# Performance work log

Measured on AMD Instinct MI355X. Metric: run time of the kernel, lower is better.

## Reference

```python
import jax, jax.numpy as jnp
import numpy as np

HIDDEN = 1024
HEADS = 16
HEAD_DIM = HIDDEN // HEADS
LN_EPS = 1e-6


def setup_inputs() -> dict:
    key = jax.random.key(0)
    ks = jax.random.split(key, 12)
    B, S, H = 2, 2048, HIDDEN
    s = 1.0 / np.sqrt(H)
    inp = {
        "hidden_states": jax.random.normal(ks[0], (B, S, H), dtype=jnp.float32),
        "attention_mask": jnp.ones((B, S), dtype=jnp.int32),
        "Wq": jax.random.normal(ks[1], (H, H), dtype=jnp.float32) * s,
        "bq": jax.random.normal(ks[2], (H,), dtype=jnp.float32) * 0.02,
        "Wk": jax.random.normal(ks[3], (H, H), dtype=jnp.float32) * s,
        "bk": jax.random.normal(ks[4], (H,), dtype=jnp.float32) * 0.02,
        "Wv": jax.random.normal(ks[5], (H, H), dtype=jnp.float32) * s,
        "bv": jax.random.normal(ks[6], (H,), dtype=jnp.float32) * 0.02,
        "Wo": jax.random.normal(ks[7], (H, H), dtype=jnp.float32) * s,
        "bo": jax.random.normal(ks[8], (H,), dtype=jnp.float32) * 0.02,
        "ln_g": jnp.ones((H,), dtype=jnp.float32),
        "ln_b": jnp.zeros((H,), dtype=jnp.float32),
    }
    return inp


def _split_heads(x):
    B, S, H = x.shape
    return x.reshape(B, S, HEADS, HEAD_DIM).transpose(0, 2, 1, 3)  # [B,h,S,d]


def reference(hidden_states, attention_mask, Wq, bq, Wk, bk, Wv, bv, Wo, bo, ln_g, ln_b):
    # torch nn.Linear: y = x @ W.T + b
    q = _split_heads(hidden_states @ Wq.T + bq)
    k = _split_heads(hidden_states @ Wk.T + bk)
    v = _split_heads(hidden_states @ Wv.T + bv)

    scores = jnp.einsum("bhqd,bhkd->bhqk", q, k) / np.sqrt(HEAD_DIM)
    # 2D mask path: [B,K] -> [B,1,1,K]; (1-mask)*-1e18 additive bias
    bias = (1.0 - attention_mask[:, None, None, :].astype(scores.dtype)) * -1e18
    probs = jax.nn.softmax(scores + bias, axis=-1)
    # dropout is identity in eval mode
    ctx = jnp.einsum("bhqk,bhkd->bhqd", probs, v)
    B, h, S, d = ctx.shape
    ctx = ctx.transpose(0, 2, 1, 3).reshape(B, S, h * d)

    out = ctx @ Wo.T + bo
    res = out + hidden_states
    mu = jnp.mean(res, axis=-1, keepdims=True)
    var = jnp.mean(jnp.square(res - mu), axis=-1, keepdims=True)
    return (res - mu) * jax.lax.rsqrt(var + LN_EPS) * ln_g + ln_b
```

## Files before the change

### kernel.cpp

```cpp
#include <hip/hip_runtime.h>
#include <hip/hip_bf16.h>

#define SEQ     2048
#define BATCH   2
#define HID     1024
#define NHEADS  16
#define HD      64
#define MTOT    4096
#define KVHALF  1024
#define LNEPS   1e-6f
#define L2E     1.4426950408889634f
#define SHIFT2  26.0f

typedef __bf16 bf16_t;
typedef bf16_t bf16x8 __attribute__((ext_vector_type(8)));
typedef bf16_t bf16x4 __attribute__((ext_vector_type(4)));
typedef short  short4v __attribute__((ext_vector_type(4)));
typedef float  floatx4 __attribute__((ext_vector_type(4)));

__device__ __forceinline__ floatx4 mfma16(bf16x8 a, bf16x8 b, floatx4 c) {
    return __builtin_amdgcn_mfma_f32_16x16x32_bf16(a, b, c, 0, 0, 0);
}
__device__ __forceinline__ floatx4 mfma16k16(bf16x4 a, bf16x4 b, floatx4 c) {
    short4v as = __builtin_bit_cast(short4v, a);
    short4v bs = __builtin_bit_cast(short4v, b);
    return __builtin_amdgcn_mfma_f32_16x16x16bf16_1k(as, bs, c, 0, 0, 0);
}
__device__ __forceinline__ bf16x8 ldg8(const bf16_t* p) { return *(const bf16x8*)p; }

__device__ __forceinline__ void glds16(const bf16_t* src, char* dst) {
    __builtin_amdgcn_global_load_lds(
        (const __attribute__((address_space(1))) unsigned int*)src,
        (__attribute__((address_space(3))) unsigned int*)dst, 16, 0, 0);
}

__device__ __forceinline__ void stage128x32(const bf16_t* __restrict__ g, int row_stride,
                                            int k0, bf16_t* lds, int wave, int lane)
{
#pragma unroll
    for (int j = 0; j < 2; j++) {
        const int rbase = wave * 32 + j * 16;
        const bf16_t* src = g + (size_t)(rbase + (lane >> 2)) * row_stride + k0 + (lane & 3) * 8;
        bf16_t* dst = lds + rbase * 32;
        __builtin_amdgcn_global_load_lds(
            (const __attribute__((address_space(1))) unsigned int*)src,
            (__attribute__((address_space(3))) unsigned int*)dst, 16, 0, 0);
    }
}
__device__ __forceinline__ void stage64x32(const bf16_t* __restrict__ g, int row_stride,
                                           int k0, bf16_t* lds, int wave, int lane)
{
    const int rbase = wave * 16;
    const bf16_t* src = g + (size_t)(rbase + (lane >> 2)) * row_stride + k0 + (lane & 3) * 8;
    bf16_t* dst = lds + rbase * 32;
    __builtin_amdgcn_global_load_lds(
        (const __attribute__((address_space(1))) unsigned int*)src,
        (__attribute__((address_space(3))) unsigned int*)dst, 16, 0, 0);
}

__global__ __launch_bounds__(256) void cvt_kernel(
    const float* sX, const float* sWq, const float* sWk, const float* sWv, const float* sWo,
    bf16_t* dX, bf16_t* dWq, bf16_t* dWk, bf16_t* dWv, bf16_t* dWo)
{
    const int z = blockIdx.z;
    const float* src; bf16_t* dst; int n;
    switch (z) {
        case 0:  src = sX;  dst = dX;  n = MTOT * HID; break;
        case 1:  src = sWq; dst = dWq; n = HID * HID;  break;
        case 2:  src = sWk; dst = dWk; n = HID * HID;  break;
        case 3:  src = sWv; dst = dWv; n = HID * HID;  break;
        default: src = sWo; dst = dWo; n = HID * HID;  break;
    }
    const int n4 = n >> 2;
    const int stride = gridDim.x * blockDim.x;
    for (int i = blockIdx.x * blockDim.x + threadIdx.x; i < n4; i += stride) {
        const float4 v = ((const float4*)src)[i];
        bf16_t o[4] = {(bf16_t)v.x, (bf16_t)v.y, (bf16_t)v.z, (bf16_t)v.w};
        *(unsigned long long*)(dst + 4 * i) = *(unsigned long long*)o;
    }
}

__global__ __launch_bounds__(256) void qkv_kernel(
    const bf16_t* __restrict__ X,
    const bf16_t* __restrict__ Wq, const float* __restrict__ bq,
    const bf16_t* __restrict__ Wk, const float* __restrict__ bk,
    const bf16_t* __restrict__ Wv, const float* __restrict__ bv,
    bf16_t* __restrict__ Qo, bf16_t* __restrict__ Ko, bf16_t* __restrict__ Vo)
{
    const int z = blockIdx.z;
    const bf16_t* W    = (z == 0) ? Wq : (z == 1) ? Wk : Wv;
    const float*  bias = (z == 0) ? bq : (z == 1) ? bk : bv;
    bf16_t*       out  = (z == 0) ? Qo : (z == 1) ? Ko : Vo;

    const int tid  = threadIdx.x;
    const int lane = tid & 63;
    const int wave = tid >> 6;
    const int l16  = lane & 15;
    const int quad = lane >> 4;
    const int m_blk = blockIdx.y * 128;
    const int n_blk = blockIdx.x * 128;
    const int m_w = (wave >> 1) * 64;
    const int n_w = (wave & 1) * 64;

    __shared__ __align__(16) char smem[18432];
    bf16_t* As = (bf16_t*)smem;
    bf16_t* Bs = (bf16_t*)(smem + 8192);

    floatx4 acc[4][4];
#pragma unroll
    for (int i = 0; i < 4; i++)
#pragma unroll
        for (int j = 0; j < 4; j++) acc[i][j] = (floatx4)0.0f;

    for (int k0 = 0; k0 < HID; k0 += 32) {
        __syncthreads();
        stage128x32(X + (size_t)m_blk * HID, HID, k0, As, wave, lane);
        stage128x32(W + (size_t)n_blk * HID, HID, k0, Bs, wave, lane);
        __syncthreads();

        bf16x8 a[4], b[4];
#pragma unroll
        for (int i = 0; i < 4; i++) a[i] = *(const bf16x8*)&As[(m_w + i * 16 + l16) * 32 + quad * 8];
#pragma unroll
        for (int j = 0; j < 4; j++) b[j] = *(const bf16x8*)&Bs[(n_w + j * 16 + l16) * 32 + quad * 8];
#pragma unroll
        for (int i = 0; i < 4; i++)
#pragma unroll
            for (int j = 0; j < 4; j++) acc[i][j] = mfma16(a[i], b[j], acc[i][j]);
    }
    __syncthreads();

    float bv_[4];
#pragma unroll
    for (int j = 0; j < 4; j++) bv_[j] = bias[n_blk + n_w + j * 16 + l16];

    bf16_t* Tw = (bf16_t*)(smem + wave * 4608);

    if (z != 2) {
        const float scale = (z == 0) ? 0.125f : 1.0f;
        const int hN = (n_blk + n_w) >> 6;
#pragma unroll
        for (int ih = 0; ih < 2; ih++) {
#pragma unroll
            for (int i2 = 0; i2 < 2; i2++) {
                const int i = ih * 2 + i2;
#pragma unroll
                for (int j = 0; j < 4; j++)
#pragma unroll
                    for (int r = 0; r < 4; r++)
                        Tw[(i2 * 16 + quad * 4 + r) * 72 + j * 16 + l16] =
                            (bf16_t)((acc[i][j][r] + bv_[j]) * scale);
            }
#pragma unroll
            for (int p = 0; p < 4; p++) {
                const int srow = p * 8 + (lane >> 3);
                const int col  = (lane & 7) * 8;
                bf16x8 v = *(const bf16x8*)&Tw[srow * 72 + col];
                const int m = m_blk + m_w + ih * 32 + srow;
                const int bb = m >> 11, s = m & (SEQ - 1);
                *(bf16x8*)&out[(((size_t)(bb * NHEADS + hN)) * SEQ + s) * HD + col] = v;
            }
        }
    } else {
        const int m0 = m_blk + m_w;
        const int bb = m0 >> 11, s0 = m0 & (SEQ - 1);
#pragma unroll
        for (int jh = 0; jh < 2; jh++) {
#pragma unroll
            for (int j2 = 0; j2 < 2; j2++) {
                const int j = jh * 2 + j2;
#pragma unroll
                for (int i = 0; i < 4; i++) {
                    bf16x4 pk;
#pragma unroll
                    for (int r = 0; r < 4; r++) pk[r] = (bf16_t)(acc[i][j][r] + bv_[j]);
                    *(bf16x4*)&Tw[(j2 * 16 + l16) * 72 + i * 16 + quad * 4] = pk;
                }
            }
#pragma unroll
            for (int p = 0; p < 4; p++) {
                const int srow = p * 8 + (lane >> 3);
                const int col  = (lane & 7) * 8;
                bf16x8 v = *(const bf16x8*)&Tw[srow * 72 + col];
                const int n = n_blk + n_w + jh * 32 + srow;
                const int h = n >> 6, d = n & 63;
                *(bf16x8*)&out[(((size_t)(bb * NHEADS + h)) * HD + d) * SEQ + s0 + col] = v;
            }
        }
    }
}

__global__ __launch_bounds__(512, 4) void attn_kernel(
    const bf16_t* __restrict__ Q, const bf16_t* __restrict__ K,
    const bf16_t* __restrict__ Vt, const int* __restrict__ mask,
    bf16_t* __restrict__ ctx)
{
    const int B   = blockIdx.x;
    const int xcd = B & 7;
    const int idx = B >> 3;
    const int bh  = xcd * 4 + (idx & 3);
    const int q0  = (idx >> 2) * 128;
    const int b   = bh >> 4;
    const int h   = bh & 15;
    const int tid  = threadIdx.x;
    const int wave = tid >> 6;
    const int wq   = wave & 3;
    const int kh   = wave >> 2;
    const int lane = tid & 63;
    const int l16  = lane & 15;
    const int quad = lane >> 4;
    const int r7   = l16 & 7;

    const bf16_t* Qh = Q  + (size_t)bh * SEQ * HD;
    const bf16_t* Kh = K  + (size_t)bh * SEQ * HD;
    const bf16_t* Vh = Vt + (size_t)bh * HD * SEQ;
    const int*    mk = mask + b * SEQ;

    __shared__ __align__(16) char smem[73728];
    char*  base  = smem + kh * 32768;
    char*  Kb0   = base;
    char*  Vb0   = base + 8192;
    char*  Kb1   = base + 16384;
    char*  Vb1   = base + 24576;
    float* bias2 = (float*)(smem + 65536);

    const int qw  = q0 + wq * 32;
    const int kvb = kh * KVHALF;

    const int srow = wq * 8 + (lane >> 3);
    const int cK   = lane & 7;
    const bf16_t* srcK = Kh + (size_t)(kvb + srow) * HD + ((cK ^ (srow & 7)) * 8);
    const bf16_t* srcV = Vh + (size_t)srow * SEQ + kvb + (((2 * cK) ^ (srow & 14)) * 4);
    const int dofs = wq * 1024;

    const int kb0 = l16 * 128 + (((quad    ) ^ r7) << 4);
    const int kb1 = l16 * 128 + (((4 + quad) ^ r7) << 4);

    glds16(srcK,                Kb0 + dofs);
    glds16(srcK + 32 * HD,      Kb0 + dofs + 4096);
    glds16(srcV,                Vb0 + dofs);
    glds16(srcV + 32 * SEQ,     Vb0 + dofs + 4096);
    for (int i = tid; i < SEQ; i += 512)
        bias2[i] = (mk[i] ? 0.0f : -1.0e30f) - SHIFT2;

    bf16x8 bQ[2][2];
#pragma unroll
    for (int qh = 0; qh < 2; qh++)
#pragma unroll
        for (int kc = 0; kc < 2; kc++)
            bQ[qh][kc] = ldg8(Qh + (size_t)(qw + qh * 16 + l16) * HD + kc * 32 + quad * 8);

    const bf16x4 onesA = {(bf16_t)1.0f, (bf16_t)1.0f, (bf16_t)1.0f, (bf16_t)1.0f};
    floatx4 O[2][4];
    floatx4 psA[2];
#pragma unroll
    for (int qh = 0; qh < 2; qh++) {
        psA[qh] = (floatx4)0.0f;
#pragma unroll
        for (int dt = 0; dt < 4; dt++) O[qh][dt] = (floatx4)0.0f;
    }

    __syncthreads();

#define STAGE(kt, KB, VB)                                            \
    do {                                                             \
        const bf16_t* sk_ = srcK + (size_t)(kt) * HD;                \
        const bf16_t* sv_ = srcV + (kt);                             \
        glds16(sk_,            (KB) + dofs);                         \
        glds16(sk_ + 32 * HD,  (KB) + dofs + 4096);                  \
        glds16(sv_,            (VB) + dofs);                         \
        glds16(sv_ + 32 * SEQ, (VB) + dofs + 4096);                  \
    } while (0)

#define COMPUTE(kt, KB, VB)                                                       \
    do {                                                                          \
        __builtin_amdgcn_s_setprio(1);                                            \
        _Pragma("unroll")                                                         \
        for (int kvt = 0; kvt < 4; kvt++) {                                       \
            bf16x8 aK0 = *(const bf16x8*)((KB) + kb0 + kvt * 2048);               \
            bf16x8 aK1 = *(const bf16x8*)((KB) + kb1 + kvt * 2048);               \
            const floatx4 ad = *(const floatx4*)&bias2[kvb + (kt) + kvt * 16 + quad * 4]; \
            bf16x4 pb[2];                                                         \
            _Pragma("unroll")                                                     \
            for (int qh = 0; qh < 2; qh++) {                                      \
                floatx4 s = (floatx4)0.0f;                                        \
                s = mfma16(aK0, bQ[qh][0], s);                                    \
                s = mfma16(aK1, bQ[qh][1], s);                                    \
                floatx4 p;                                                        \
                _Pragma("unroll")                                                 \
                for (int r = 0; r < 4; r++)                                       \
                    p[r] = __builtin_amdgcn_exp2f(fmaf(s[r], L2E, ad[r]));        \
                _Pragma("unroll")                                                 \
                for (int r = 0; r < 4; r++) pb[qh][r] = (bf16_t)p[r];             \
            }                                                                     \
            psA[0] = mfma16k16(onesA, pb[0], psA[0]);                             \
            psA[1] = mfma16k16(onesA, pb[1], psA[1]);                             \
            const int vofs = l16 * 128 + ((((kvt << 2) + quad) ^ (l16 & 14)) << 3); \
            _Pragma("unroll")                                                     \
            for (int dt = 0; dt < 4; dt++) {                                      \
                bf16x4 aV = *(const bf16x4*)((VB) + vofs + dt * 2048);            \
                O[0][dt] = mfma16k16(aV, pb[0], O[0][dt]);                        \
                O[1][dt] = mfma16k16(aV, pb[1], O[1][dt]);                        \
            }                                                                     \
        }                                                                         \
        __builtin_amdgcn_s_setprio(0);                                            \
    } while (0)

    for (int t = 0; t < 16; t += 2) {
        STAGE((t + 1) * 64, Kb1, Vb1);
        COMPUTE(t * 64, Kb0, Vb0);
        __syncthreads();
        if (t + 2 < 16) STAGE((t + 2) * 64, Kb0, Vb0);
        COMPUTE((t + 1) * 64, Kb1, Vb1);
        __syncthreads();
    }
#undef STAGE
#undef COMPUTE

    if (kh == 1) {
        float* mw = (float*)(smem + wq * 10240) + lane * 40;
#pragma unroll
        for (int qh = 0; qh < 2; qh++) {
#pragma unroll
            for (int dt = 0; dt < 4; dt++)
                *(floatx4*)(mw + qh * 16 + dt * 4) = O[qh][dt];
            *(floatx4*)(mw + 32 + qh * 4) = psA[qh];
        }
    }
    __syncthreads();
    if (kh == 1) return;

    {
        const float* mr = (const float*)(smem + wq * 10240) + lane * 40;
#pragma unroll
        for (int qh = 0; qh < 2; qh++) {
#pragma unroll
            for (int dt = 0; dt < 4; dt++)
                O[qh][dt] += *(const floatx4*)(mr + qh * 16 + dt * 4);
            psA[qh] += *(const floatx4*)(mr + 32 + qh * 4);
        }
    }

#pragma unroll
    for (int qh = 0; qh < 2; qh++) {
        const float su = psA[qh][0];
        const float linv = (su > 0.0f) ? 1.0f / su : 0.0f;

        bf16_t* Pw = (bf16_t*)(smem + wq * 10240 + qh * 2304);
#pragma unroll
        for (int dt = 0; dt < 4; dt++) {
            floatx4 o = O[qh][dt] * linv;
            bf16x4 pk;
#pragma unroll
            for (int r = 0; r < 4; r++) pk[r] = (bf16_t)o[r];
            *(bf16x4*)&Pw[l16 * 72 + dt * 16 + quad * 4] = pk;
        }
#pragma unroll
        for (int ch = 0; ch < 2; ch++) {
            const int cc  = ch * 64 + lane;
            const int row = cc >> 3;
            const int col = (cc & 7) * 8;
            bf16x8 vv = *(const bf16x8*)&Pw[row * 72 + col];
            *(bf16x8*)&ctx[((size_t)(b * SEQ + qw + qh * 16 + row)) * HID + h * 64 + col] = vv;
        }
    }
}

__global__ __launch_bounds__(256) void oproj_kernel(
    const bf16_t* __restrict__ C, const bf16_t* __restrict__ Wo,
    const float* __restrict__ bo, const float* __restrict__ X,
    float* __restrict__ res)
{
    const int tid  = threadIdx.x;
    const int lane = tid & 63;
    const int wave = tid >> 6;
    const int l16  = lane & 15;
    const int quad = lane >> 4;
    const int m_blk = blockIdx.y * 64;
    const int n_blk = blockIdx.x * 128;
    const int n_w   = wave * 32;

    __shared__ __align__(16) char smem[12288];
    bf16_t* As = (bf16_t*)smem;
    bf16_t* Bs = (bf16_t*)(smem + 4096);

    floatx4 acc[4][2];
#pragma unroll
    for (int i = 0; i < 4; i++)
#pragma unroll
        for (int j = 0; j < 2; j++) acc[i][j] = (floatx4)0.0f;

    for (int k0 = 0; k0 < HID; k0 += 32) {
        __syncthreads();
        stage64x32 (C  + (size_t)m_blk * HID, HID, k0, As, wave, lane);
        stage128x32(Wo + (size_t)n_blk * HID, HID, k0, Bs, wave, lane);
        __syncthreads();

        bf16x8 a[4], b[2];
#pragma unroll
        for (int i = 0; i < 4; i++) a[i] = *(const bf16x8*)&As[(i * 16 + l16) * 32 + quad * 8];
#pragma unroll
        for (int j = 0; j < 2; j++) b[j] = *(const bf16x8*)&Bs[(n_w + j * 16 + l16) * 32 + quad * 8];
#pragma unroll
        for (int i = 0; i < 4; i++)
#pragma unroll
            for (int j = 0; j < 2; j++) acc[i][j] = mfma16(a[i], b[j], acc[i][j]);
    }
    __syncthreads();

    float bv_[2];
#pragma unroll
    for (int j = 0; j < 2; j++) bv_[j] = bo[n_blk + n_w + j * 16 + l16];

    float* Tw = (float*)(smem + wave * 2304);
#pragma unroll
    for (int ch = 0; ch < 4; ch++) {
#pragma unroll
        for (int j = 0; j < 2; j++)
#pragma unroll
            for (int r = 0; r < 4; r++)
                Tw[(quad * 4 + r) * 36 + j * 16 + l16] = acc[ch][j][r] + bv_[j];
#pragma unroll
        for (int cc = 0; cc < 2; cc++) {
            const int idx = cc * 64 + lane;
            const int row = idx >> 3;
            const int col = (idx & 7) * 4;
            float4 v = *(const float4*)&Tw[row * 36 + col];
            const int m = m_blk + ch * 16 + row;
            const float4 xv = *(const float4*)&X[(size_t)m * HID + n_blk + n_w + col];
            v.x += xv.x; v.y += xv.y; v.z += xv.z; v.w += xv.w;
            *(float4*)&res[(size_t)m * HID + n_blk + n_w + col] = v;
        }
    }
}

__global__ __launch_bounds__(256) void ln_kernel(
    const float* __restrict__ res,
    const float* __restrict__ g, const float* __restrict__ be,
    float* __restrict__ out)
{
    __shared__ float red1[4], red2[4];
    const int row  = blockIdx.x;
    const int lane = threadIdx.x & 63;
    const int wave = threadIdx.x >> 6;
    const float4 v = ((const float4*)(res + (size_t)row * HID))[threadIdx.x];

    float s = v.x + v.y + v.z + v.w;
#pragma unroll
    for (int off = 1; off < 64; off <<= 1) s += __shfl_xor(s, off, 64);
    if (lane == 0) red1[wave] = s;
    __syncthreads();
    const float mu = (red1[0] + red1[1] + red1[2] + red1[3]) * (1.0f / HID);

    const float d0 = v.x - mu, d1 = v.y - mu, d2 = v.z - mu, d3 = v.w - mu;
    float ss = d0 * d0 + d1 * d1 + d2 * d2 + d3 * d3;
#pragma unroll
    for (int off = 1; off < 64; off <<= 1) ss += __shfl_xor(ss, off, 64);
    if (lane == 0) red2[wave] = ss;
    __syncthreads();
    const float var = (red2[0] + red2[1] + red2[2] + red2[3]) * (1.0f / HID);
    const float rstd = rsqrtf(var + LNEPS);

    const float4 gv = ((const float4*)g)[threadIdx.x];
    const float4 bv = ((const float4*)be)[threadIdx.x];
    float4 o;
    o.x = d0 * rstd * gv.x + bv.x;
    o.y = d1 * rstd * gv.y + bv.y;
    o.z = d2 * rstd * gv.z + bv.z;
    o.w = d3 * rstd * gv.w + bv.w;
    ((float4*)(out + (size_t)row * HID))[threadIdx.x] = o;
}

extern "C" void kernel_launch(void* const* d_in, const int* in_sizes, int n_in,
                              void* d_out, int out_size, void* d_ws, size_t ws_size,
                              hipStream_t stream)
{
    const float* X  = (const float*)d_in[0];
    const int* mask = (const int*)d_in[1];
    const float* Wq = (const float*)d_in[2];  const float* bq = (const float*)d_in[3];
    const float* Wk = (const float*)d_in[4];  const float* bk = (const float*)d_in[5];
    const float* Wv = (const float*)d_in[6];  const float* bv = (const float*)d_in[7];
    const float* Wo = (const float*)d_in[8];  const float* bo = (const float*)d_in[9];
    const float* g  = (const float*)d_in[10]; const float* be = (const float*)d_in[11];
    float* out = (float*)d_out;

    char* ws = (char*)d_ws;
    bf16_t* Qb  = (bf16_t*)(ws);
    bf16_t* Kb  = (bf16_t*)(ws + (8ull  << 20));
    bf16_t* Vb  = (bf16_t*)(ws + (16ull << 20));
    bf16_t* Cb  = (bf16_t*)(ws + (24ull << 20));
    float*  Rb  = (float*)(ws);
    bf16_t* Xc  = (bf16_t*)(ws + (32ull << 20));
    bf16_t* Wqc = (bf16_t*)(ws + (40ull << 20));
    bf16_t* Wkc = (bf16_t*)(ws + (42ull << 20));
    bf16_t* Wvc = (bf16_t*)(ws + (44ull << 20));
    bf16_t* Woc = (bf16_t*)(ws + (46ull << 20));

    cvt_kernel <<<dim3(512, 1, 5), 256, 0, stream>>>(X, Wq, Wk, Wv, Wo, Xc, Wqc, Wkc, Wvc, Woc);
    qkv_kernel <<<dim3(8, 32, 3), 256, 0, stream>>>(Xc, Wqc, bq, Wkc, bk, Wvc, bv, Qb, Kb, Vb);
    attn_kernel<<<dim3(512), 512, 0, stream>>>(Qb, Kb, Vb, mask, Cb);
    oproj_kernel<<<dim3(8, 64), 256, 0, stream>>>(Cb, Woc, bo, X, Rb);
    ln_kernel  <<<MTOT, 256, 0, stream>>>(Rb, g, be, out);
}
```

Before: 121.1 us.

## Drop intra-block split-KV in attention; four waves each scan full sequence

The attention kernel previously used 8 waves per block, with two groups each covering half of the KV range and merging partial O and row sums through shared memory. Now each block has 4 waves that each loop over the whole KV sequence, with smaller shared memory and no merge step. This removes the merge traffic and the extra barrier, and lowers LDS use per block. With the grid size unchanged, it halves the waves per CU and doubles the serial loop length, which risks losing latency hiding.

New measurement: 122.6 us. Within noise of the previous version (+1.2%).

```diff
diff --git a/kernel.cpp b/kernel.cpp
--- a/kernel.cpp
+++ b/kernel.cpp
@@ -7,7 +7,6 @@
 #define NHEADS  16
 #define HD      64
 #define MTOT    4096
-#define KVHALF  1024
 #define LNEPS   1e-6f
 #define L2E     1.4426950408889634f
 #define SHIFT2  26.0f
@@ -190,7 +189,7 @@
     }
 }
 
-__global__ __launch_bounds__(512, 4) void attn_kernel(
+__global__ __launch_bounds__(256, 4) void attn_kernel(
     const bf16_t* __restrict__ Q, const bf16_t* __restrict__ K,
     const bf16_t* __restrict__ Vt, const int* __restrict__ mask,
     bf16_t* __restrict__ ctx)
@@ -204,8 +203,6 @@
     const int h   = bh & 15;
     const int tid  = threadIdx.x;
     const int wave = tid >> 6;
-    const int wq   = wave & 3;
-    const int kh   = wave >> 2;
     const int lane = tid & 63;
     const int l16  = lane & 15;
     const int quad = lane >> 4;
@@ -216,31 +213,29 @@
     const bf16_t* Vh = Vt + (size_t)bh * HD * SEQ;
     const int*    mk = mask + b * SEQ;
 
-    __shared__ __align__(16) char smem[73728];
-    char*  base  = smem + kh * 32768;
-    char*  Kb0   = base;
-    char*  Vb0   = base + 8192;
-    char*  Kb1   = base + 16384;
-    char*  Vb1   = base + 24576;
-    float* bias2 = (float*)(smem + 65536);
-
-    const int qw  = q0 + wq * 32;
-    const int kvb = kh * KVHALF;
-
-    const int srow = wq * 8 + (lane >> 3);
-    const int cK   = lane & 7;
-    const bf16_t* srcK = Kh + (size_t)(kvb + srow) * HD + ((cK ^ (srow & 7)) * 8);
-    const bf16_t* srcV = Vh + (size_t)srow * SEQ + kvb + (((2 * cK) ^ (srow & 14)) * 4);
-    const int dofs = wq * 1024;
+    __shared__ __align__(16) char smem[40960];
+    char*  Kb0   = smem;
+    char*  Vb0   = smem + 8192;
+    char*  Kb1   = smem + 16384;
+    char*  Vb1   = smem + 24576;
+    float* bias2 = (float*)(smem + 32768);
+
+    const int qw = q0 + wave * 32;
+
+    const int srow = tid >> 3;
+    const int cK   = tid & 7;
+    const bf16_t* srcK = Kh + (size_t)srow * HD + ((cK ^ (srow & 7)) * 8);
+    const bf16_t* srcV = Vh + (size_t)srow * SEQ + (((2 * cK) ^ (srow & 14)) * 4);
+    const int dofs = wave * 1024;
 
     const int kb0 = l16 * 128 + (((quad    ) ^ r7) << 4);
     const int kb1 = l16 * 128 + (((4 + quad) ^ r7) << 4);
 
-    glds16(srcK,                Kb0 + dofs);
-    glds16(srcK + 32 * HD,      Kb0 + dofs + 4096);
-    glds16(srcV,                Vb0 + dofs);
-    glds16(srcV + 32 * SEQ,     Vb0 + dofs + 4096);
-    for (int i = tid; i < SEQ; i += 512)
+    glds16(srcK,            Kb0 + dofs);
+    glds16(srcK + 32 * HD,  Kb0 + dofs + 4096);
+    glds16(srcV,            Vb0 + dofs);
+    glds16(srcV + 32 * SEQ, Vb0 + dofs + 4096);
+    for (int i = tid; i < SEQ; i += 256)
         bias2[i] = (mk[i] ? 0.0f : -1.0e30f) - SHIFT2;
 
     bf16x8 bQ[2][2];
@@ -279,7 +274,7 @@
         for (int kvt = 0; kvt < 4; kvt++) {                                       \
             bf16x8 aK0 = *(const bf16x8*)((KB) + kb0 + kvt * 2048);               \
             bf16x8 aK1 = *(const bf16x8*)((KB) + kb1 + kvt * 2048);               \
-            const floatx4 ad = *(const floatx4*)&bias2[kvb + (kt) + kvt * 16 + quad * 4]; \
+            const floatx4 ad = *(const floatx4*)&bias2[(kt) + kvt * 16 + quad * 4]; \
             bf16x4 pb[2];                                                         \
             _Pragma("unroll")                                                     \
             for (int qh = 0; qh < 2; qh++) {                                      \
@@ -306,47 +301,23 @@
         __builtin_amdgcn_s_setprio(0);                                            \
     } while (0)
 
-    for (int t = 0; t < 16; t += 2) {
+    for (int t = 0; t < 32; t += 2) {
         STAGE((t + 1) * 64, Kb1, Vb1);
         COMPUTE(t * 64, Kb0, Vb0);
         __syncthreads();
-        if (t + 2 < 16) STAGE((t + 2) * 64, Kb0, Vb0);
+        if (t + 2 < 32) STAGE((t + 2) * 64, Kb0, Vb0);
         COMPUTE((t + 1) * 64, Kb1, Vb1);
         __syncthreads();
     }
 #undef STAGE
 #undef COMPUTE
-
-    if (kh == 1) {
-        float* mw = (float*)(smem + wq * 10240) + lane * 40;
-#pragma unroll
-        for (int qh = 0; qh < 2; qh++) {
-#pragma unroll
-            for (int dt = 0; dt < 4; dt++)
-                *(floatx4*)(mw + qh * 16 + dt * 4) = O[qh][dt];
-            *(floatx4*)(mw + 32 + qh * 4) = psA[qh];
-        }
-    }
-    __syncthreads();
-    if (kh == 1) return;
-
-    {
-        const float* mr = (const float*)(smem + wq * 10240) + lane * 40;
-#pragma unroll
-        for (int qh = 0; qh < 2; qh++) {
-#pragma unroll
-            for (int dt = 0; dt < 4; dt++)
-                O[qh][dt] += *(const floatx4*)(mr + qh * 16 + dt * 4);
-            psA[qh] += *(const floatx4*)(mr + 32 + qh * 4);
-        }
-    }
 
 #pragma unroll
     for (int qh = 0; qh < 2; qh++) {
         const float su = psA[qh][0];
         const float linv = (su > 0.0f) ? 1.0f / su : 0.0f;
 
-        bf16_t* Pw = (bf16_t*)(smem + wq * 10240 + qh * 2304);
+        bf16_t* Pw = (bf16_t*)(smem + wave * 4608 + qh * 2304);
 #pragma unroll
         for (int dt = 0; dt < 4; dt++) {
             floatx4 o = O[qh][dt] * linv;
@@ -498,7 +469,7 @@
 
     cvt_kernel <<<dim3(512, 1, 5), 256, 0, stream>>>(X, Wq, Wk, Wv, Wo, Xc, Wqc, Wkc, Wvc, Woc);
     qkv_kernel <<<dim3(8, 32, 3), 256, 0, stream>>>(Xc, Wqc, bq, Wkc, bk, Wvc, bv, Qb, Kb, Vb);
-    attn_kernel<<<dim3(512), 512, 0, stream>>>(Qb, Kb, Vb, mask, Cb);
+    attn_kernel<<<dim3(512), 256, 0, stream>>>(Qb, Kb, Vb, mask, Cb);
     oproj_kernel<<<dim3(8, 64), 256, 0, stream>>>(Cb, Woc, bo, X, Rb);
     ln_kernel  <<<MTOT, 256, 0, stream>>>(Rb, g, be, out);
 }
```
